# Kernel tuning notes

Hardware: AMD Instinct MI355X
Metric: run time of the kernel (lower is better)

The kernel has to match this reference:

```python
import jax, jax.numpy as jnp
import numpy as np

B, Q, D, H, HD, P = 1, 2048, 2048, 16, 128, 512


def setup_inputs() -> dict:
    key = jax.random.key(0)
    ks = jax.random.split(key, 12)
    x = jax.random.normal(ks[0], (B, Q, D), jnp.float32)
    prefix_key = jax.random.normal(ks[1], (B, P, H, HD), jnp.float32)
    prefix_value = jax.random.normal(ks[2], (B, P, H, HD), jnp.float32)
    s = 1.0 / np.sqrt(D)
    Wq = jax.random.normal(ks[3], (D, H, HD), jnp.float32) * s
    Wk = jax.random.normal(ks[4], (D, H, HD), jnp.float32) * s
    Wv = jax.random.normal(ks[5], (D, H, HD), jnp.float32) * s
    bq = jnp.zeros((H, HD), jnp.float32)
    bk = jnp.zeros((H, HD), jnp.float32)
    bv = jnp.zeros((H, HD), jnp.float32)
    prefix_gate = jax.random.normal(ks[6], (H,), jnp.float32) * 0.1
    Wout = jax.random.normal(ks[7], (H, HD, D), jnp.float32) * (1.0 / np.sqrt(D))
    bout = jnp.zeros((D,), jnp.float32)
    # prefix fully visible, causal mask over the suffix (current sequence)
    causal = jnp.tril(jnp.ones((Q, Q), bool))
    mask = jnp.concatenate([jnp.ones((Q, P), bool), causal], axis=1)[None, None]  # [1,1,Q,P+Q]
    return dict(x=x, prefix_key=prefix_key, prefix_value=prefix_value,
                Wq=Wq, bq=bq, Wk=Wk, bk=bk, Wv=Wv, bv=bv,
                prefix_gate=prefix_gate, Wout=Wout, bout=bout, mask=mask)


def reference(x, prefix_key, prefix_value, Wq, bq, Wk, bk, Wv, bv, prefix_gate, Wout, bout, mask):
    head_dim = Wq.shape[-1]
    pl = prefix_key.shape[1]
    q = jnp.einsum('bqd,dhk->bqhk', x, Wq) + bq   # [B,Q,H,HD]
    k = jnp.einsum('bqd,dhk->bqhk', x, Wk) + bk
    v = jnp.einsum('bqd,dhk->bqhk', x, Wv) + bv
    k = jnp.concatenate([prefix_key, k], axis=1)   # [B,P+Q,H,HD]
    v = jnp.concatenate([prefix_value, v], axis=1)
    q = q / jnp.sqrt(jnp.asarray(head_dim, q.dtype))
    w = jnp.einsum('bqhd,bkhd->bhqk', q, k)        # [B,H,Q,P+Q]
    big_neg = jnp.finfo(w.dtype).min
    w = jnp.where(mask, w, big_neg)
    gate = prefix_gate[None, :, None, None]
    w_prefix = jax.nn.softmax(w[..., :pl]) * gate   # gated prefix segment
    w_suffix = jax.nn.softmax(w[..., pl:])          # regular suffix softmax
    w = jnp.concatenate([w_prefix, w_suffix], axis=-1)
    o = jnp.einsum('bhqk,bkhd->bqhd', w, v)         # [B,Q,H,HD]
    return jnp.einsum('bqhd,hdo->bqo', o, Wout) + bout
```

## Files before the change

### kernel.cpp

```cpp
#include <hip/hip_runtime.h>
#include <hip/hip_bf16.h>

typedef __bf16 bf16x8 __attribute__((ext_vector_type(8)));
typedef __bf16 bf16x4v __attribute__((ext_vector_type(4)));
typedef float f32x4 __attribute__((ext_vector_type(4)));

#define DMODEL 2048
#define NH 16
#define HD 128
#define PLEN 512
#define QLEN 2048
#define KVLEN 2560

__device__ __forceinline__ void gload_lds16(const void* g, void* l) {
  __builtin_amdgcn_global_load_lds((const __attribute__((address_space(1))) void*)g,
                                   (__attribute__((address_space(3))) void*)l, 16, 0, 0);
}


__global__ __launch_bounds__(256) void k_transpose_bf16(const float* __restrict__ in,
                                                        __bf16* __restrict__ out) {
  __shared__ float tile[64][65];
  const int t = threadIdx.x;
  const int tx = t & 63, ty = t >> 6;
  const int r0 = blockIdx.y * 64, c0 = blockIdx.x * 64;
#pragma unroll
  for (int i = 0; i < 16; ++i) {
    int r = ty + i * 4;
    tile[r][tx] = in[(size_t)(r0 + r) * DMODEL + c0 + tx];
  }
  __syncthreads();
#pragma unroll
  for (int i = 0; i < 16; ++i) {
    int r = ty + i * 4;
    out[(size_t)(c0 + r) * DMODEL + r0 + tx] = (__bf16)tile[tx][r];
  }
}

__global__ __launch_bounds__(256) void k_f32_to_bf16(const float* __restrict__ in,
                                                     __bf16* __restrict__ out, int n4) {
  int i = blockIdx.x * blockDim.x + threadIdx.x;
  int stride = gridDim.x * blockDim.x;
  for (; i < n4; i += stride) {
    float4 v = ((const float4*)in)[i];
    bf16x4v o;
    o[0] = (__bf16)v.x; o[1] = (__bf16)v.y; o[2] = (__bf16)v.z; o[3] = (__bf16)v.w;
    ((bf16x4v*)out)[i] = o;
  }
}

__global__ __launch_bounds__(256) void k_prefix(const float* __restrict__ pk,
                                                const float* __restrict__ pv,
                                                __bf16* __restrict__ Kall,
                                                __bf16* __restrict__ VT) {
  int idx = blockIdx.x * 256 + threadIdx.x;
  int hd = idx & 127;
  int h = (idx >> 7) & 15;
  int p = idx >> 11;
  Kall[(size_t)h * KVLEN * HD + (size_t)p * HD + hd] = (__bf16)pk[idx];
  VT[(size_t)h * HD * KVLEN + (size_t)hd * KVLEN + p] = (__bf16)pv[idx];
}


template <int BN>
__device__ __forceinline__ void stage_tile(const __bf16* __restrict__ A,
                                           const __bf16* __restrict__ BT,
                                           char* AsmB, char* BsmB,
                                           int m0, int n0, int k0, int w, int l) {
#pragma unroll
  for (int i = 0; i < 2; ++i) {
    int base = i * 4096 + w * 1024;
    int o = base + l * 16;
    int row = o >> 6, col = (o & 63) >> 1;
    gload_lds16(A + (size_t)(m0 + row) * DMODEL + k0 + col, AsmB + base);
  }
  if constexpr (BN == 128) {
#pragma unroll
    for (int i = 0; i < 2; ++i) {
      int base = i * 4096 + w * 1024;
      int o = base + l * 16;
      int row = o >> 6, col = (o & 63) >> 1;
      gload_lds16(BT + (size_t)(n0 + row) * DMODEL + k0 + col, BsmB + base);
    }
  } else {
    int base = w * 1024;
    int o = base + l * 16;
    int row = o >> 6, col = (o & 63) >> 1;
    gload_lds16(BT + (size_t)(n0 + row) * DMODEL + k0 + col, BsmB + base);
  }
}

template <int BN>
__device__ __forceinline__ void gemm_mainloop_db(const __bf16* __restrict__ A,
                                                 const __bf16* __restrict__ BT,
                                                 __bf16* Asm, __bf16* Bsm,
                                                 int m0, int n0, int w, int l,
                                                 f32x4 (&acc)[4][BN / 32]) {
  constexpr int NI = BN / 32;
  constexpr int ABUF = 4096;
  constexpr int BBUF = BN * 32;
  const int lr = l & 15, lg = l >> 4;
  int cur = 0;
  stage_tile<BN>(A, BT, (char*)Asm, (char*)Bsm, m0, n0, 0, w, l);
  __syncthreads();
  for (int k0 = 0; k0 < DMODEL; k0 += 32) {
    if (k0 + 32 < DMODEL)
      stage_tile<BN>(A, BT, (char*)(Asm + (cur ^ 1) * ABUF), (char*)(Bsm + (cur ^ 1) * BBUF),
                     m0, n0, k0 + 32, w, l);
    const __bf16* Ab = Asm + cur * ABUF;
    const __bf16* Bb = Bsm + cur * BBUF;
    bf16x8 af[4], bfv[NI];
#pragma unroll
    for (int mi = 0; mi < 4; ++mi)
      af[mi] = *(const bf16x8*)(Ab + ((w >> 1) * 64 + mi * 16 + lr) * 32 + lg * 8);
#pragma unroll
    for (int ni = 0; ni < NI; ++ni)
      bfv[ni] = *(const bf16x8*)(Bb + ((w & 1) * (BN / 2) + ni * 16 + lr) * 32 + lg * 8);
    __builtin_amdgcn_s_setprio(1);
#pragma unroll
    for (int mi = 0; mi < 4; ++mi)
#pragma unroll
      for (int ni = 0; ni < NI; ++ni)
        acc[mi][ni] = __builtin_amdgcn_mfma_f32_16x16x32_bf16(af[mi], bfv[ni], acc[mi][ni], 0, 0, 0);
    __builtin_amdgcn_s_setprio(0);
    __syncthreads();
    cur ^= 1;
  }
}

__global__ __launch_bounds__(256) void gemm_qkv(const __bf16* __restrict__ xb,
                                                const __bf16* __restrict__ WqT,
                                                const __bf16* __restrict__ WkT,
                                                const __bf16* __restrict__ WvT,
                                                const float* __restrict__ bq,
                                                const float* __restrict__ bk,
                                                const float* __restrict__ bv,
                                                __bf16* __restrict__ Qs,
                                                __bf16* __restrict__ Kall,
                                                __bf16* __restrict__ VT) {
  __shared__ __bf16 Asm[2][4096];
  __shared__ __bf16 Bsm[2][4096];
  const int t = threadIdx.x, w = t >> 6, l = t & 63;
  const int m0 = blockIdx.x * 128, n0 = blockIdx.y * 128;
  const int z = blockIdx.z;
  const __bf16* BT = (z == 0) ? WqT : ((z == 1) ? WkT : WvT);
  const float* bias = (z == 0) ? bq : ((z == 1) ? bk : bv);
  f32x4 acc[4][4];
#pragma unroll
  for (int mi = 0; mi < 4; ++mi)
#pragma unroll
    for (int ni = 0; ni < 4; ++ni) acc[mi][ni] = (f32x4){0.f, 0.f, 0.f, 0.f};
  gemm_mainloop_db<128>(xb, BT, &Asm[0][0], &Bsm[0][0], m0, n0, w, l, acc);
  const int lr = l & 15, lg = l >> 4;
#pragma unroll
  for (int mi = 0; mi < 4; ++mi)
#pragma unroll
    for (int ni = 0; ni < 4; ++ni)
#pragma unroll
      for (int r = 0; r < 4; ++r) {
        int row = m0 + (w >> 1) * 64 + mi * 16 + lg * 4 + r;
        int col = n0 + (w & 1) * 64 + ni * 16 + lr;
        float v = acc[mi][ni][r] + bias[col];
        int hh = col >> 7, hd = col & 127;
        if (z == 0) {
          Qs[(size_t)hh * QLEN * HD + (size_t)row * HD + hd] = (__bf16)(v * 0.08838834764831845f);
        } else if (z == 1) {
          Kall[(size_t)hh * KVLEN * HD + (size_t)(PLEN + row) * HD + hd] = (__bf16)v;
        } else {
          VT[(size_t)hh * HD * KVLEN + (size_t)hd * KVLEN + (PLEN + row)] = (__bf16)v;
        }
      }
}

__global__ __launch_bounds__(256) void gemm_out(const __bf16* __restrict__ Ob,
                                                const __bf16* __restrict__ WoT,
                                                const float* __restrict__ bout,
                                                float* __restrict__ out) {
  __shared__ __bf16 Asm[2][4096];
  __shared__ __bf16 Bsm[2][2048];
  const int t = threadIdx.x, w = t >> 6, l = t & 63;
  const int m0 = blockIdx.x * 128, n0 = blockIdx.y * 64;
  f32x4 acc[4][2];
#pragma unroll
  for (int mi = 0; mi < 4; ++mi)
#pragma unroll
    for (int ni = 0; ni < 2; ++ni) acc[mi][ni] = (f32x4){0.f, 0.f, 0.f, 0.f};
  gemm_mainloop_db<64>(Ob, WoT, &Asm[0][0], &Bsm[0][0], m0, n0, w, l, acc);
  const int lr = l & 15, lg = l >> 4;
#pragma unroll
  for (int mi = 0; mi < 4; ++mi)
#pragma unroll
    for (int ni = 0; ni < 2; ++ni)
#pragma unroll
      for (int r = 0; r < 4; ++r) {
        int row = m0 + (w >> 1) * 64 + mi * 16 + lg * 4 + r;
        int col = n0 + (w & 1) * 32 + ni * 16 + lr;
        out[(size_t)row * DMODEL + col] = acc[mi][ni][r] + bout[col];
      }
}

__global__ __launch_bounds__(256, 2) void k_attn(const __bf16* __restrict__ Qs,
                                                 const __bf16* __restrict__ Kall,
                                                 const __bf16* __restrict__ VT,
                                                 const float* __restrict__ gate,
                                                 __bf16* __restrict__ Ob) {
  __shared__ __bf16 Ksm[2][4096];
  __shared__ __bf16 Vsm[2][4096];
  __shared__ __bf16 Pl[4][16 * 40];
  const int h = blockIdx.y;
  const int qt = (h < 8) ? blockIdx.x : (31 - blockIdx.x);
  const int t = threadIdx.x, w = t >> 6, l = t & 63;
  const int lr = l & 15, lg = l >> 4;
  const int q0 = qt * 64 + w * 16;
  const __bf16* Qh = Qs + (size_t)h * QLEN * HD;
  const char* Khb = (const char*)(Kall + (size_t)h * KVLEN * HD);
  const char* Vhb = (const char*)(VT + (size_t)h * HD * KVLEN);
  __bf16* Pw = &Pl[w][0];

  bf16x8 qf[4];
#pragma unroll
  for (int c = 0; c < 4; ++c)
    qf[c] = *(const bf16x8*)(Qh + (size_t)(q0 + lr) * HD + c * 32 + lg * 8);

  f32x4 acc1[8], acc2[8];
  float ss1[4], ss2[4];
#pragma unroll
  for (int c = 0; c < 8; ++c) {
    acc1[c] = (f32x4){0.f, 0.f, 0.f, 0.f};
    acc2[c] = (f32x4){0.f, 0.f, 0.f, 0.f};
  }
#pragma unroll
  for (int r = 0; r < 4; ++r) { ss1[r] = 0.f; ss2[r] = 0.f; }

  auto STAGE = [&](int buf, int kb) {
#pragma unroll
    for (int i = 0; i < 2; ++i) {
      int o = (i * 256 + w * 64 + l) * 16;
      int po = o ^ (((o >> 8) & 7) << 4);
      gload_lds16(Khb + (size_t)kb * 256 + po, (char*)&Ksm[buf][0] + i * 4096 + w * 1024);
    }
#pragma unroll
    for (int i = 0; i < 2; ++i) {
      int o = (i * 256 + w * 64 + l) * 16;
      int po = o ^ (((o >> 7) & 7) << 4);
      int row = po >> 6, colb = po & 63;
      gload_lds16(Vhb + (size_t)row * (KVLEN * 2) + (size_t)kb * 2 + colb,
                  (char*)&Vsm[buf][0] + i * 4096 + w * 1024);
    }
  };

  auto COMPUTE = [&](int buf, int mrel, bool domask, f32x4 (&ACC)[8], float (&SS)[4]) {
    const char* Kb = (const char*)&Ksm[buf][0];
    const char* Vb = (const char*)&Vsm[buf][0];
    f32x4 st0 = {0.f, 0.f, 0.f, 0.f}, st1 = {0.f, 0.f, 0.f, 0.f};
    __builtin_amdgcn_s_setprio(1);
#pragma unroll
    for (int c = 0; c < 4; ++c) {
      int o0 = lr * 256 + c * 64 + lg * 16;        o0 ^= ((o0 >> 8) & 7) << 4;
      int o1 = (16 + lr) * 256 + c * 64 + lg * 16; o1 ^= ((o1 >> 8) & 7) << 4;
      bf16x8 kf0 = *(const bf16x8*)(Kb + o0);
      bf16x8 kf1 = *(const bf16x8*)(Kb + o1);
      st0 = __builtin_amdgcn_mfma_f32_16x16x32_bf16(qf[c], kf0, st0, 0, 0, 0);
      st1 = __builtin_amdgcn_mfma_f32_16x16x32_bf16(qf[c], kf1, st1, 0, 0, 0);
    }
    __builtin_amdgcn_s_setprio(0);
#pragma unroll
    for (int r = 0; r < 4; ++r) {
      if (domask) {
        int qq = q0 + lg * 4 + r;
        if (mrel + lr > qq) st0[r] = -1e30f;
        if (mrel + 16 + lr > qq) st1[r] = -1e30f;
      }
      float p0 = __expf(st0[r] - 16.0f);
      float p1 = __expf(st1[r] - 16.0f);
      SS[r] += p0 + p1;
      Pw[(lg * 4 + r) * 40 + lr] = (__bf16)p0;
      Pw[(lg * 4 + r) * 40 + 16 + lr] = (__bf16)p1;
    }
    bf16x8 pf = *(const bf16x8*)(Pw + lr * 40 + lg * 8);
    __builtin_amdgcn_s_setprio(1);
#pragma unroll
    for (int c = 0; c < 8; ++c) {
      int o = (c * 16 + lr) * 64 + lg * 16; o ^= ((o >> 7) & 7) << 4;
      bf16x8 vf = *(const bf16x8*)(Vb + o);
      ACC[c] = __builtin_amdgcn_mfma_f32_16x16x32_bf16(pf, vf, ACC[c], 0, 0, 0);
    }
    __builtin_amdgcn_s_setprio(0);
  };

  int cur = 0;
  STAGE(0, 0);
  __syncthreads();
#pragma unroll 1
  for (int i = 0; i < PLEN / 32; ++i) {
    if (i + 1 < PLEN / 32) STAGE(cur ^ 1, (i + 1) * 32);
    COMPUTE(cur, 0, false, acc1, ss1);
    __syncthreads();
    cur ^= 1;
  }

  const int ntb = 2 * qt + 2;
  cur = 0;
  STAGE(0, PLEN);
  __syncthreads();
#pragma unroll 1
  for (int i = 0; i < ntb; ++i) {
    if (i + 1 < ntb) STAGE(cur ^ 1, PLEN + (i + 1) * 32);
    COMPUTE(cur, i * 32, i * 32 + 31 > q0, acc2, ss2);
    __syncthreads();
    cur ^= 1;
  }

  const float g = gate[h];
#pragma unroll
  for (int r = 0; r < 4; ++r) {
    float s1 = ss1[r];
    s1 += __shfl_xor(s1, 1); s1 += __shfl_xor(s1, 2);
    s1 += __shfl_xor(s1, 4); s1 += __shfl_xor(s1, 8);
    float s2 = ss2[r];
    s2 += __shfl_xor(s2, 1); s2 += __shfl_xor(s2, 2);
    s2 += __shfl_xor(s2, 4); s2 += __shfl_xor(s2, 8);
    const float f1 = g / s1;
    const float f2 = 1.0f / s2;
    const int qrow = q0 + lg * 4 + r;
#pragma unroll
    for (int c = 0; c < 8; ++c) {
      float val = acc1[c][r] * f1 + acc2[c][r] * f2;
      Ob[(size_t)qrow * DMODEL + h * HD + c * 16 + lr] = (__bf16)val;
    }
  }
}


extern "C" void kernel_launch(void* const* d_in, const int* in_sizes, int n_in,
                              void* d_out, int out_size, void* d_ws, size_t ws_size,
                              hipStream_t stream) {
  const float* x    = (const float*)d_in[0];
  const float* pk   = (const float*)d_in[1];
  const float* pv   = (const float*)d_in[2];
  const float* Wq   = (const float*)d_in[3];
  const float* bq   = (const float*)d_in[4];
  const float* Wk   = (const float*)d_in[5];
  const float* bk   = (const float*)d_in[6];
  const float* Wv   = (const float*)d_in[7];
  const float* bv   = (const float*)d_in[8];
  const float* gate = (const float*)d_in[9];
  const float* Wout = (const float*)d_in[10];
  const float* bout = (const float*)d_in[11];
  float* out = (float*)d_out;

  char* ws = (char*)d_ws;
  size_t off = 0;
  auto alc = [&](size_t bytes) -> char* {
    char* p = ws + off;
    off += bytes;
    off = (off + 255) & ~(size_t)255;
    return p;
  };
  __bf16* xb   = (__bf16*)alc((size_t)DMODEL * DMODEL * 2);
  __bf16* WqT  = (__bf16*)alc((size_t)DMODEL * DMODEL * 2);
  __bf16* WkT  = (__bf16*)alc((size_t)DMODEL * DMODEL * 2);
  __bf16* WvT  = (__bf16*)alc((size_t)DMODEL * DMODEL * 2);
  __bf16* WoT  = (__bf16*)alc((size_t)DMODEL * DMODEL * 2);
  __bf16* Qs   = (__bf16*)alc((size_t)NH * QLEN * HD * 2);
  __bf16* Kall = (__bf16*)alc((size_t)NH * KVLEN * HD * 2);
  __bf16* VTa  = (__bf16*)alc((size_t)NH * HD * KVLEN * 2);
  __bf16* Ob   = (__bf16*)alc((size_t)QLEN * DMODEL * 2);

  dim3 tgrid(32, 32);
  k_transpose_bf16<<<tgrid, 256, 0, stream>>>(Wq, WqT);
  k_transpose_bf16<<<tgrid, 256, 0, stream>>>(Wk, WkT);
  k_transpose_bf16<<<tgrid, 256, 0, stream>>>(Wv, WvT);
  k_transpose_bf16<<<tgrid, 256, 0, stream>>>(Wout, WoT);
  k_f32_to_bf16<<<1024, 256, 0, stream>>>(x, xb, (DMODEL * DMODEL) / 4);
  k_prefix<<<4096, 256, 0, stream>>>(pk, pv, Kall, VTa);

  gemm_qkv<<<dim3(16, 16, 3), 256, 0, stream>>>(xb, WqT, WkT, WvT, bq, bk, bv, Qs, Kall, VTa);
  k_attn<<<dim3(32, 16), 256, 0, stream>>>(Qs, Kall, VTa, gate, Ob);
  gemm_out<<<dim3(16, 32), 256, 0, stream>>>(Ob, WoT, bout, out);
}
```

Measured before the change: 221.1 us.

## Triple-buffer GEMM and attention loads with vmcnt waits and XCD-aware block remap

Replaces double buffering with a three-stage LDS ring in the GEMM mainloop and the attention kernel. Loads are issued two tiles ahead, and explicit s_waitcnt vmcnt counts plus raw barriers replace __syncthreads. The attention prefix and suffix loops are merged into one pipelined loop so there is no pipeline drain between them. Grids are flattened to 1D and block IDs are remapped so blocks sharing data land on the same XCD, which should improve L2 reuse. The costs are more LDS per block, which may lower occupancy, and hand-tuned vmcnt values that must match the exact number of loads issued per stage.

```diff
diff --git a/kernel.cpp b/kernel.cpp
--- a/kernel.cpp
+++ b/kernel.cpp
@@ -11,6 +11,9 @@
 #define PLEN 512
 #define QLEN 2048
 #define KVLEN 2560
+
+#define FENCE() asm volatile("" ::: "memory")
+#define LGKM0() asm volatile("s_waitcnt lgkmcnt(0)" ::: "memory")
 
 __device__ __forceinline__ void gload_lds16(const void* g, void* l) {
   __builtin_amdgcn_global_load_lds((const __attribute__((address_space(1))) void*)g,
@@ -100,13 +103,21 @@
   constexpr int ABUF = 4096;
   constexpr int BBUF = BN * 32;
   const int lr = l & 15, lg = l >> 4;
+  stage_tile<BN>(A, BT, (char*)Asm, (char*)Bsm, m0, n0, 0, w, l);
+  stage_tile<BN>(A, BT, (char*)(Asm + ABUF), (char*)(Bsm + BBUF), m0, n0, 32, w, l);
   int cur = 0;
-  stage_tile<BN>(A, BT, (char*)Asm, (char*)Bsm, m0, n0, 0, w, l);
-  __syncthreads();
   for (int k0 = 0; k0 < DMODEL; k0 += 32) {
-    if (k0 + 32 < DMODEL)
-      stage_tile<BN>(A, BT, (char*)(Asm + (cur ^ 1) * ABUF), (char*)(Bsm + (cur ^ 1) * BBUF),
-                     m0, n0, k0 + 32, w, l);
+    int k2 = k0 + 64;
+    if (k2 > DMODEL - 32) k2 = DMODEL - 32;
+    int nxt = cur + 2; if (nxt >= 3) nxt -= 3;
+    stage_tile<BN>(A, BT, (char*)(Asm + nxt * ABUF), (char*)(Bsm + nxt * BBUF),
+                   m0, n0, k2, w, l);
+    if constexpr (BN == 128) {
+      asm volatile("s_waitcnt vmcnt(8)" ::: "memory");
+    } else {
+      asm volatile("s_waitcnt vmcnt(6)" ::: "memory");
+    }
+    FENCE(); __builtin_amdgcn_s_barrier(); FENCE();
     const __bf16* Ab = Asm + cur * ABUF;
     const __bf16* Bb = Bsm + cur * BBUF;
     bf16x8 af[4], bfv[NI];
@@ -123,8 +134,9 @@
       for (int ni = 0; ni < NI; ++ni)
         acc[mi][ni] = __builtin_amdgcn_mfma_f32_16x16x32_bf16(af[mi], bfv[ni], acc[mi][ni], 0, 0, 0);
     __builtin_amdgcn_s_setprio(0);
-    __syncthreads();
-    cur ^= 1;
+    LGKM0();
+    FENCE(); __builtin_amdgcn_s_barrier(); FENCE();
+    cur = cur + 1; if (cur >= 3) cur -= 3;
   }
 }
 
@@ -138,11 +150,14 @@
                                                 __bf16* __restrict__ Qs,
                                                 __bf16* __restrict__ Kall,
                                                 __bf16* __restrict__ VT) {
-  __shared__ __bf16 Asm[2][4096];
-  __shared__ __bf16 Bsm[2][4096];
+  __shared__ __bf16 Asm[3][4096];
+  __shared__ __bf16 Bsm[3][4096];
   const int t = threadIdx.x, w = t >> 6, l = t & 63;
-  const int m0 = blockIdx.x * 128, n0 = blockIdx.y * 128;
-  const int z = blockIdx.z;
+  const int id = blockIdx.x;
+  const int id2 = (id & 7) * 96 + (id >> 3);
+  const int z = id2 >> 8;
+  const int rem = id2 & 255;
+  const int m0 = (rem & 15) * 128, n0 = (rem >> 4) * 128;
   const __bf16* BT = (z == 0) ? WqT : ((z == 1) ? WkT : WvT);
   const float* bias = (z == 0) ? bq : ((z == 1) ? bk : bv);
   f32x4 acc[4][4];
@@ -176,10 +191,12 @@
                                                 const __bf16* __restrict__ WoT,
                                                 const float* __restrict__ bout,
                                                 float* __restrict__ out) {
-  __shared__ __bf16 Asm[2][4096];
-  __shared__ __bf16 Bsm[2][2048];
+  __shared__ __bf16 Asm[3][4096];
+  __shared__ __bf16 Bsm[3][2048];
   const int t = threadIdx.x, w = t >> 6, l = t & 63;
-  const int m0 = blockIdx.x * 128, n0 = blockIdx.y * 64;
+  const int id = blockIdx.x;
+  const int id2 = (id & 7) * 64 + (id >> 3);
+  const int m0 = (id2 & 15) * 128, n0 = (id2 >> 4) * 64;
   f32x4 acc[4][2];
 #pragma unroll
   for (int mi = 0; mi < 4; ++mi)
@@ -204,11 +221,13 @@
                                                  const __bf16* __restrict__ VT,
                                                  const float* __restrict__ gate,
                                                  __bf16* __restrict__ Ob) {
-  __shared__ __bf16 Ksm[2][4096];
-  __shared__ __bf16 Vsm[2][4096];
+  __shared__ __bf16 Ksm[3][4096];
+  __shared__ __bf16 Vsm[3][4096];
   __shared__ __bf16 Pl[4][16 * 40];
-  const int h = blockIdx.y;
-  const int qt = (h < 8) ? blockIdx.x : (31 - blockIdx.x);
+  const int id2 = (blockIdx.x & 7) * 64 + (blockIdx.x >> 3);
+  const int h = id2 >> 5;
+  const int bx = id2 & 31;
+  const int qt = (h & 1) ? (31 - bx) : bx;
   const int t = threadIdx.x, w = t >> 6, l = t & 63;
   const int lr = l & 15, lg = l >> 4;
   const int q0 = qt * 64 + w * 16;
@@ -288,27 +307,26 @@
     __builtin_amdgcn_s_setprio(0);
   };
 
+  const int NT = 16 + 2 * qt + 2;
+  STAGE(0, 0);
+  STAGE(1, 32);
   int cur = 0;
-  STAGE(0, 0);
-  __syncthreads();
 #pragma unroll 1
-  for (int i = 0; i < PLEN / 32; ++i) {
-    if (i + 1 < PLEN / 32) STAGE(cur ^ 1, (i + 1) * 32);
-    COMPUTE(cur, 0, false, acc1, ss1);
-    __syncthreads();
-    cur ^= 1;
-  }
-
-  const int ntb = 2 * qt + 2;
-  cur = 0;
-  STAGE(0, PLEN);
-  __syncthreads();
-#pragma unroll 1
-  for (int i = 0; i < ntb; ++i) {
-    if (i + 1 < ntb) STAGE(cur ^ 1, PLEN + (i + 1) * 32);
-    COMPUTE(cur, i * 32, i * 32 + 31 > q0, acc2, ss2);
-    __syncthreads();
-    cur ^= 1;
+  for (int i = 0; i < NT; ++i) {
+    int it = i + 2; if (it > NT - 1) it = NT - 1;
+    int nxt = cur + 2; if (nxt >= 3) nxt -= 3;
+    STAGE(nxt, it * 32);
+    asm volatile("s_waitcnt vmcnt(8)" ::: "memory");
+    FENCE(); __builtin_amdgcn_s_barrier(); FENCE();
+    if (i < 16) {
+      COMPUTE(cur, 0, false, acc1, ss1);
+    } else {
+      const int mrel = (i - 16) * 32;
+      COMPUTE(cur, mrel, mrel + 31 > q0, acc2, ss2);
+    }
+    LGKM0();
+    FENCE(); __builtin_amdgcn_s_barrier(); FENCE();
+    cur = cur + 1; if (cur >= 3) cur -= 3;
   }
 
   const float g = gate[h];
@@ -375,7 +393,7 @@
   k_f32_to_bf16<<<1024, 256, 0, stream>>>(x, xb, (DMODEL * DMODEL) / 4);
   k_prefix<<<4096, 256, 0, stream>>>(pk, pv, Kall, VTa);
 
-  gemm_qkv<<<dim3(16, 16, 3), 256, 0, stream>>>(xb, WqT, WkT, WvT, bq, bk, bv, Qs, Kall, VTa);
-  k_attn<<<dim3(32, 16), 256, 0, stream>>>(Qs, Kall, VTa, gate, Ob);
-  gemm_out<<<dim3(16, 32), 256, 0, stream>>>(Ob, WoT, bout, out);
-}
+  gemm_qkv<<<768, 256, 0, stream>>>(xb, WqT, WkT, WvT, bq, bk, bv, Qs, Kall, VTa);
+  k_attn<<<512, 256, 0, stream>>>(Qs, Kall, VTa, gate, Ob);
+  gemm_out<<<512, 256, 0, stream>>>(Ob, WoT, bout, out);
+}
```

New measurement: 243.7 us. 1.1x slower.

## Triple-buffer attention K/V staging, overlap next QK with softmax-PV, batch transposes

Applied to the files above, without the earlier changes.

The attention kernel moves from double to triple-buffered LDS staging and merges the prefix and suffix loops into one pipelined loop. The QK MFMA for tile i+1 is issued before the softmax and PV for tile i, and explicit vmcnt waits replace __syncthreads so loads stay in flight. The four weight transposes are also merged into a single launch using blockIdx.z. This costs more LDS per block, which may limit occupancy, and the hand-written waitcnt and barrier ordering is fragile.

```diff
diff --git a/kernel.cpp b/kernel.cpp
--- a/kernel.cpp
+++ b/kernel.cpp
@@ -12,15 +12,27 @@
 #define QLEN 2048
 #define KVLEN 2560
 
+#define FENCE() asm volatile("" ::: "memory")
+#define LGKM0() asm volatile("s_waitcnt lgkmcnt(0)" ::: "memory")
+
 __device__ __forceinline__ void gload_lds16(const void* g, void* l) {
   __builtin_amdgcn_global_load_lds((const __attribute__((address_space(1))) void*)g,
                                    (__attribute__((address_space(3))) void*)l, 16, 0, 0);
 }
 
 
-__global__ __launch_bounds__(256) void k_transpose_bf16(const float* __restrict__ in,
-                                                        __bf16* __restrict__ out) {
+__global__ __launch_bounds__(256) void k_transpose4(const float* __restrict__ s0,
+                                                    const float* __restrict__ s1,
+                                                    const float* __restrict__ s2,
+                                                    const float* __restrict__ s3,
+                                                    __bf16* __restrict__ d0,
+                                                    __bf16* __restrict__ d1,
+                                                    __bf16* __restrict__ d2,
+                                                    __bf16* __restrict__ d3) {
   __shared__ float tile[64][65];
+  const int z = blockIdx.z;
+  const float* in = (z == 0) ? s0 : (z == 1) ? s1 : (z == 2) ? s2 : s3;
+  __bf16* out = (z == 0) ? d0 : (z == 1) ? d1 : (z == 2) ? d2 : d3;
   const int t = threadIdx.x;
   const int tx = t & 63, ty = t >> 6;
   const int r0 = blockIdx.y * 64, c0 = blockIdx.x * 64;
@@ -204,8 +216,8 @@
                                                  const __bf16* __restrict__ VT,
                                                  const float* __restrict__ gate,
                                                  __bf16* __restrict__ Ob) {
-  __shared__ __bf16 Ksm[2][4096];
-  __shared__ __bf16 Vsm[2][4096];
+  __shared__ __bf16 Ksm[3][4096];
+  __shared__ __bf16 Vsm[3][4096];
   __shared__ __bf16 Pl[4][16 * 40];
   const int h = blockIdx.y;
   const int qt = (h < 8) ? blockIdx.x : (31 - blockIdx.x);
@@ -249,10 +261,10 @@
     }
   };
 
-  auto COMPUTE = [&](int buf, int mrel, bool domask, f32x4 (&ACC)[8], float (&SS)[4]) {
+  auto QK = [&](int buf, f32x4& s0, f32x4& s1) {
     const char* Kb = (const char*)&Ksm[buf][0];
-    const char* Vb = (const char*)&Vsm[buf][0];
-    f32x4 st0 = {0.f, 0.f, 0.f, 0.f}, st1 = {0.f, 0.f, 0.f, 0.f};
+    s0 = (f32x4){0.f, 0.f, 0.f, 0.f};
+    s1 = (f32x4){0.f, 0.f, 0.f, 0.f};
     __builtin_amdgcn_s_setprio(1);
 #pragma unroll
     for (int c = 0; c < 4; ++c) {
@@ -260,19 +272,24 @@
       int o1 = (16 + lr) * 256 + c * 64 + lg * 16; o1 ^= ((o1 >> 8) & 7) << 4;
       bf16x8 kf0 = *(const bf16x8*)(Kb + o0);
       bf16x8 kf1 = *(const bf16x8*)(Kb + o1);
-      st0 = __builtin_amdgcn_mfma_f32_16x16x32_bf16(qf[c], kf0, st0, 0, 0, 0);
-      st1 = __builtin_amdgcn_mfma_f32_16x16x32_bf16(qf[c], kf1, st1, 0, 0, 0);
+      s0 = __builtin_amdgcn_mfma_f32_16x16x32_bf16(qf[c], kf0, s0, 0, 0, 0);
+      s1 = __builtin_amdgcn_mfma_f32_16x16x32_bf16(qf[c], kf1, s1, 0, 0, 0);
     }
     __builtin_amdgcn_s_setprio(0);
+  };
+
+  auto SMPV = [&](int buf, f32x4 s0, f32x4 s1, int mrel, bool domask,
+                  f32x4 (&ACC)[8], float (&SS)[4]) {
+    const char* Vb = (const char*)&Vsm[buf][0];
 #pragma unroll
     for (int r = 0; r < 4; ++r) {
       if (domask) {
         int qq = q0 + lg * 4 + r;
-        if (mrel + lr > qq) st0[r] = -1e30f;
-        if (mrel + 16 + lr > qq) st1[r] = -1e30f;
+        if (mrel + lr > qq) s0[r] = -1e30f;
+        if (mrel + 16 + lr > qq) s1[r] = -1e30f;
       }
-      float p0 = __expf(st0[r] - 16.0f);
-      float p1 = __expf(st1[r] - 16.0f);
+      float p0 = __expf(s0[r] - 16.0f);
+      float p1 = __expf(s1[r] - 16.0f);
       SS[r] += p0 + p1;
       Pw[(lg * 4 + r) * 40 + lr] = (__bf16)p0;
       Pw[(lg * 4 + r) * 40 + 16 + lr] = (__bf16)p1;
@@ -288,27 +305,34 @@
     __builtin_amdgcn_s_setprio(0);
   };
 
-  int cur = 0;
+  const int NT = 16 + 2 * qt + 2;
   STAGE(0, 0);
-  __syncthreads();
+  STAGE(1, 32);
+  asm volatile("s_waitcnt vmcnt(4)" ::: "memory");
+  FENCE(); __builtin_amdgcn_s_barrier(); FENCE();
+  f32x4 stA, stB;
+  QK(0, stA, stB);
 #pragma unroll 1
-  for (int i = 0; i < PLEN / 32; ++i) {
-    if (i + 1 < PLEN / 32) STAGE(cur ^ 1, (i + 1) * 32);
-    COMPUTE(cur, 0, false, acc1, ss1);
-    __syncthreads();
-    cur ^= 1;
-  }
-
-  const int ntb = 2 * qt + 2;
-  cur = 0;
-  STAGE(0, PLEN);
-  __syncthreads();
-#pragma unroll 1
-  for (int i = 0; i < ntb; ++i) {
-    if (i + 1 < ntb) STAGE(cur ^ 1, PLEN + (i + 1) * 32);
-    COMPUTE(cur, i * 32, i * 32 + 31 > q0, acc2, ss2);
-    __syncthreads();
-    cur ^= 1;
+  for (int i = 0; i < NT; ++i) {
+    int it = i + 2; if (it > NT - 1) it = NT - 1;
+    int b2 = i + 2; while (b2 >= 3) b2 -= 3;
+    STAGE(b2, it * 32);
+    asm volatile("s_waitcnt vmcnt(4)" ::: "memory");
+    FENCE(); __builtin_amdgcn_s_barrier(); FENCE();
+    f32x4 c0 = stA, c1 = stB;
+    if (i + 1 < NT) {
+      int b1 = i + 1; while (b1 >= 3) b1 -= 3;
+      QK(b1, stA, stB);
+    }
+    int b0 = i; while (b0 >= 3) b0 -= 3;
+    if (i < 16) {
+      SMPV(b0, c0, c1, 0, false, acc1, ss1);
+    } else {
+      const int mrel = (i - 16) * 32;
+      SMPV(b0, c0, c1, mrel, mrel + 31 > q0, acc2, ss2);
+    }
+    LGKM0();
+    FENCE(); __builtin_amdgcn_s_barrier(); FENCE();
   }
 
   const float g = gate[h];
@@ -367,11 +391,7 @@
   __bf16* VTa  = (__bf16*)alc((size_t)NH * HD * KVLEN * 2);
   __bf16* Ob   = (__bf16*)alc((size_t)QLEN * DMODEL * 2);
 
-  dim3 tgrid(32, 32);
-  k_transpose_bf16<<<tgrid, 256, 0, stream>>>(Wq, WqT);
-  k_transpose_bf16<<<tgrid, 256, 0, stream>>>(Wk, WkT);
-  k_transpose_bf16<<<tgrid, 256, 0, stream>>>(Wv, WvT);
-  k_transpose_bf16<<<tgrid, 256, 0, stream>>>(Wout, WoT);
+  k_transpose4<<<dim3(32, 32, 4), 256, 0, stream>>>(Wq, Wk, Wv, Wout, WqT, WkT, WvT, WoT);
   k_f32_to_bf16<<<1024, 256, 0, stream>>>(x, xb, (DMODEL * DMODEL) / 4);
   k_prefix<<<4096, 256, 0, stream>>>(pk, pv, Kall, VTa);
 
```

New measurement: 223.2 us. No clear change (+0.9%).

## Split attention over KV into partial blocks with separate combine kernel

Applied to the files above, without the earlier changes.

The attention kernel now splits each query tile's KV range across KS=2 blocks, with interleaved 32-key tiles per split. Each split writes its unnormalized bf16 partial outputs and row sums to workspace, and a new combine kernel sums the partials, applies the gate and both softmax normalizations, and writes Ob. The grid grows to 1024 blocks with launch bounds raised to 4 per CU, and the prefix stage prefetches the first suffix tile. The four weight transposes are merged into one launch. The cost is extra global traffic for the partial buffers, one more kernel launch, and rounding from storing partial accumulators as bf16.

```diff
diff --git a/kernel.cpp b/kernel.cpp
--- a/kernel.cpp
+++ b/kernel.cpp
@@ -18,9 +18,18 @@
 }
 
 
-__global__ __launch_bounds__(256) void k_transpose_bf16(const float* __restrict__ in,
-                                                        __bf16* __restrict__ out) {
+__global__ __launch_bounds__(256) void k_transpose4(const float* __restrict__ s0,
+                                                    const float* __restrict__ s1,
+                                                    const float* __restrict__ s2,
+                                                    const float* __restrict__ s3,
+                                                    __bf16* __restrict__ d0,
+                                                    __bf16* __restrict__ d1,
+                                                    __bf16* __restrict__ d2,
+                                                    __bf16* __restrict__ d3) {
   __shared__ float tile[64][65];
+  const int z = blockIdx.z;
+  const float* in = (z == 0) ? s0 : (z == 1) ? s1 : (z == 2) ? s2 : s3;
+  __bf16* out = (z == 0) ? d0 : (z == 1) ? d1 : (z == 2) ? d2 : d3;
   const int t = threadIdx.x;
   const int tx = t & 63, ty = t >> 6;
   const int r0 = blockIdx.y * 64, c0 = blockIdx.x * 64;
@@ -199,16 +208,29 @@
       }
 }
 
-__global__ __launch_bounds__(256, 2) void k_attn(const __bf16* __restrict__ Qs,
+template <int KS>
+__global__ __launch_bounds__(256, 4) void k_attn(const __bf16* __restrict__ Qs,
                                                  const __bf16* __restrict__ Kall,
                                                  const __bf16* __restrict__ VT,
-                                                 const float* __restrict__ gate,
-                                                 __bf16* __restrict__ Ob) {
+                                                 __bf16* __restrict__ P1buf,
+                                                 float* __restrict__ S1buf,
+                                                 __bf16* __restrict__ P2buf,
+                                                 float* __restrict__ S2buf) {
   __shared__ __bf16 Ksm[2][4096];
   __shared__ __bf16 Vsm[2][4096];
   __shared__ __bf16 Pl[4][16 * 40];
-  const int h = blockIdx.y;
-  const int qt = (h < 8) ? blockIdx.x : (31 - blockIdx.x);
+  const int id = blockIdx.x;
+  const int b = id & 255, k = id >> 8;
+  const int h = b >> 4, m = b & 15;
+  int qt, z;
+  if constexpr (KS == 2) {
+    z = k >> 1;
+    const int j = 2 * m + (k >> 1);
+    qt = (k & 1) ? (31 - j) : j;
+  } else {
+    z = 0;
+    qt = (k & 1) ? (31 - 2 * m) : (2 * m);
+  }
   const int t = threadIdx.x, w = t >> 6, l = t & 63;
   const int lr = l & 15, lg = l >> 4;
   const int q0 = qt * 64 + w * 16;
@@ -222,15 +244,8 @@
   for (int c = 0; c < 4; ++c)
     qf[c] = *(const bf16x8*)(Qh + (size_t)(q0 + lr) * HD + c * 32 + lg * 8);
 
-  f32x4 acc1[8], acc2[8];
-  float ss1[4], ss2[4];
-#pragma unroll
-  for (int c = 0; c < 8; ++c) {
-    acc1[c] = (f32x4){0.f, 0.f, 0.f, 0.f};
-    acc2[c] = (f32x4){0.f, 0.f, 0.f, 0.f};
-  }
-#pragma unroll
-  for (int r = 0; r < 4; ++r) { ss1[r] = 0.f; ss2[r] = 0.f; }
+  f32x4 acc[8];
+  float ss[4];
 
   auto STAGE = [&](int buf, int kb) {
 #pragma unroll
@@ -249,7 +264,7 @@
     }
   };
 
-  auto COMPUTE = [&](int buf, int mrel, bool domask, f32x4 (&ACC)[8], float (&SS)[4]) {
+  auto COMPUTE = [&](int buf, int mrel, bool domask) {
     const char* Kb = (const char*)&Ksm[buf][0];
     const char* Vb = (const char*)&Vsm[buf][0];
     f32x4 st0 = {0.f, 0.f, 0.f, 0.f}, st1 = {0.f, 0.f, 0.f, 0.f};
@@ -273,7 +288,7 @@
       }
       float p0 = __expf(st0[r] - 16.0f);
       float p1 = __expf(st1[r] - 16.0f);
-      SS[r] += p0 + p1;
+      ss[r] += p0 + p1;
       Pw[(lg * 4 + r) * 40 + lr] = (__bf16)p0;
       Pw[(lg * 4 + r) * 40 + 16 + lr] = (__bf16)p1;
     }
@@ -283,52 +298,81 @@
     for (int c = 0; c < 8; ++c) {
       int o = (c * 16 + lr) * 64 + lg * 16; o ^= ((o >> 7) & 7) << 4;
       bf16x8 vf = *(const bf16x8*)(Vb + o);
-      ACC[c] = __builtin_amdgcn_mfma_f32_16x16x32_bf16(pf, vf, ACC[c], 0, 0, 0);
+      acc[c] = __builtin_amdgcn_mfma_f32_16x16x32_bf16(pf, vf, acc[c], 0, 0, 0);
     }
     __builtin_amdgcn_s_setprio(0);
   };
 
+  auto STORE_PHASE = [&](__bf16* PBUF, float* SBUF) {
+    const size_t rb = (size_t)(z * NH + h) * QLEN;
+#pragma unroll
+    for (int r = 0; r < 4; ++r) {
+      float s = ss[r];
+      s += __shfl_xor(s, 1); s += __shfl_xor(s, 2);
+      s += __shfl_xor(s, 4); s += __shfl_xor(s, 8);
+      const int row = q0 + lg * 4 + r;
+      if (lr == 0) SBUF[rb + row] = s;
+#pragma unroll
+      for (int c = 0; c < 8; ++c)
+        PBUF[(rb + row) * HD + c * 16 + lr] = (__bf16)acc[c][r];
+    }
+  };
+
+#pragma unroll
+  for (int c = 0; c < 8; ++c) acc[c] = (f32x4){0.f, 0.f, 0.f, 0.f};
+#pragma unroll
+  for (int r = 0; r < 4; ++r) ss[r] = 0.f;
   int cur = 0;
-  STAGE(0, 0);
+  STAGE(0, z * 32);
   __syncthreads();
 #pragma unroll 1
-  for (int i = 0; i < PLEN / 32; ++i) {
-    if (i + 1 < PLEN / 32) STAGE(cur ^ 1, (i + 1) * 32);
-    COMPUTE(cur, 0, false, acc1, ss1);
+  for (int tt = z; tt < 16; tt += KS) {
+    if (tt + KS < 16) STAGE(cur ^ 1, (tt + KS) * 32);
+    else STAGE(cur ^ 1, PLEN + z * 32);
+    COMPUTE(cur, 0, false);
     __syncthreads();
     cur ^= 1;
   }
-
+  STORE_PHASE(P1buf, S1buf);
+
+#pragma unroll
+  for (int c = 0; c < 8; ++c) acc[c] = (f32x4){0.f, 0.f, 0.f, 0.f};
+#pragma unroll
+  for (int r = 0; r < 4; ++r) ss[r] = 0.f;
   const int ntb = 2 * qt + 2;
-  cur = 0;
-  STAGE(0, PLEN);
-  __syncthreads();
 #pragma unroll 1
-  for (int i = 0; i < ntb; ++i) {
-    if (i + 1 < ntb) STAGE(cur ^ 1, PLEN + (i + 1) * 32);
-    COMPUTE(cur, i * 32, i * 32 + 31 > q0, acc2, ss2);
+  for (int tt = z; tt < ntb; tt += KS) {
+    if (tt + KS < ntb) STAGE(cur ^ 1, PLEN + (tt + KS) * 32);
+    COMPUTE(cur, tt * 32, tt * 32 + 31 > q0);
     __syncthreads();
     cur ^= 1;
   }
-
-  const float g = gate[h];
-#pragma unroll
-  for (int r = 0; r < 4; ++r) {
-    float s1 = ss1[r];
-    s1 += __shfl_xor(s1, 1); s1 += __shfl_xor(s1, 2);
-    s1 += __shfl_xor(s1, 4); s1 += __shfl_xor(s1, 8);
-    float s2 = ss2[r];
-    s2 += __shfl_xor(s2, 1); s2 += __shfl_xor(s2, 2);
-    s2 += __shfl_xor(s2, 4); s2 += __shfl_xor(s2, 8);
-    const float f1 = g / s1;
-    const float f2 = 1.0f / s2;
-    const int qrow = q0 + lg * 4 + r;
-#pragma unroll
-    for (int c = 0; c < 8; ++c) {
-      float val = acc1[c][r] * f1 + acc2[c][r] * f2;
-      Ob[(size_t)qrow * DMODEL + h * HD + c * 16 + lr] = (__bf16)val;
-    }
-  }
+  STORE_PHASE(P2buf, S2buf);
+}
+
+template <int KS>
+__global__ __launch_bounds__(256) void k_combine(const __bf16* __restrict__ P1buf,
+                                                 const float* __restrict__ S1buf,
+                                                 const __bf16* __restrict__ P2buf,
+                                                 const float* __restrict__ S2buf,
+                                                 const float* __restrict__ gate,
+                                                 __bf16* __restrict__ Ob) {
+  const int idx = blockIdx.x * 256 + threadIdx.x;
+  const int d = idx & 127;
+  const int q = (idx >> 7) & 2047;
+  const int h = idx >> 18;
+  const size_t rq = (size_t)h * QLEN + q;
+  float a1 = 0.f, a2 = 0.f, s1 = 0.f, s2 = 0.f;
+#pragma unroll
+  for (int zz = 0; zz < KS; ++zz) {
+    const size_t zb = (size_t)zz * NH * QLEN;
+    a1 += (float)P1buf[(zb + rq) * HD + d];
+    a2 += (float)P2buf[(zb + rq) * HD + d];
+    s1 += S1buf[zb + rq];
+    s2 += S2buf[zb + rq];
+  }
+  float o = a1 * (gate[h] / s1) + a2 / s2;
+  Ob[(size_t)q * DMODEL + h * HD + d] = (__bf16)o;
 }
 
 
@@ -367,15 +411,27 @@
   __bf16* VTa  = (__bf16*)alc((size_t)NH * HD * KVLEN * 2);
   __bf16* Ob   = (__bf16*)alc((size_t)QLEN * DMODEL * 2);
 
-  dim3 tgrid(32, 32);
-  k_transpose_bf16<<<tgrid, 256, 0, stream>>>(Wq, WqT);
-  k_transpose_bf16<<<tgrid, 256, 0, stream>>>(Wk, WkT);
-  k_transpose_bf16<<<tgrid, 256, 0, stream>>>(Wv, WvT);
-  k_transpose_bf16<<<tgrid, 256, 0, stream>>>(Wout, WoT);
+  const size_t per_split = (size_t)NH * QLEN * HD * 2 * 2
+                         + (size_t)NH * QLEN * 4 * 2 + 1024;
+  int KS = (off + 2 * per_split <= ws_size) ? 2 : 1;
+  __bf16* P1buf = (__bf16*)alc((size_t)KS * NH * QLEN * HD * 2);
+  __bf16* P2buf = (__bf16*)alc((size_t)KS * NH * QLEN * HD * 2);
+  float*  S1buf = (float*)alc((size_t)KS * NH * QLEN * 4);
+  float*  S2buf = (float*)alc((size_t)KS * NH * QLEN * 4);
+
+  k_transpose4<<<dim3(32, 32, 4), 256, 0, stream>>>(Wq, Wk, Wv, Wout, WqT, WkT, WvT, WoT);
   k_f32_to_bf16<<<1024, 256, 0, stream>>>(x, xb, (DMODEL * DMODEL) / 4);
   k_prefix<<<4096, 256, 0, stream>>>(pk, pv, Kall, VTa);
 
   gemm_qkv<<<dim3(16, 16, 3), 256, 0, stream>>>(xb, WqT, WkT, WvT, bq, bk, bv, Qs, Kall, VTa);
-  k_attn<<<dim3(32, 16), 256, 0, stream>>>(Qs, Kall, VTa, gate, Ob);
+
+  const int ncomb = (NH * QLEN * HD) / 256;
+  if (KS == 2) {
+    k_attn<2><<<1024, 256, 0, stream>>>(Qs, Kall, VTa, P1buf, S1buf, P2buf, S2buf);
+    k_combine<2><<<ncomb, 256, 0, stream>>>(P1buf, S1buf, P2buf, S2buf, gate, Ob);
+  } else {
+    k_attn<1><<<512, 256, 0, stream>>>(Qs, Kall, VTa, P1buf, S1buf, P2buf, S2buf);
+    k_combine<1><<<ncomb, 256, 0, stream>>>(P1buf, S1buf, P2buf, S2buf, gate, Ob);
+  }
   gemm_out<<<dim3(16, 32), 256, 0, stream>>>(Ob, WoT, bout, out);
 }
```

Result: faster. 195.0 us (-11.8%).
